# Kernel optimization log

Measured on AMD Instinct MI355X. Metric: run time of the kernel, lower is better.

The kernel has to match this reference:

```python
import jax, jax.numpy as jnp
import numpy as np

CLAMP_MIN, CLAMP_MAX = -3.0, 3.0
RANK = 16


def setup_inputs() -> dict:
    key = jax.random.key(0)
    ks = jax.random.split(key, 8)
    B, N, D, H, R = 8, 4096, 1024, 256, RANK
    s = 0.02  # small weight std so clamp/exp are well-conditioned
    return {
        "query_emb": jax.random.normal(ks[0], (B, D), jnp.float32),
        "context_embs": jax.random.normal(ks[1], (B, N, D), jnp.float32),
        "W1": jax.random.normal(ks[2], (D, H), jnp.float32) * s,
        "b1": jnp.zeros((H,), jnp.float32),
        "Wd": jax.random.normal(ks[3], (H, D), jnp.float32) * s,
        "bd": jnp.zeros((D,), jnp.float32),
        "WL": jax.random.normal(ks[4], (H, D * R), jnp.float32) * s,
        "bL": jnp.zeros((D * R,), jnp.float32),
        "Wdel": jax.random.normal(ks[5], (H, D), jnp.float32) * s,
        "bdel": jnp.zeros((D,), jnp.float32),
        "Wa": jax.random.normal(ks[6], (H, D), jnp.float32) * s,
        "ba": jnp.zeros((D,), jnp.float32),
    }


def reference(query_emb, context_embs, W1, b1, Wd, bd, WL, bL, Wdel, bdel, Wa, ba):
    B, N, D = context_embs.shape
    R = RANK
    # Backbone: Linear + ReLU (assumed MLP backbone)
    h = jax.nn.relu(query_emb @ W1 + b1)                      # (B,H)
    # Parameter heads (SkewGaussian.forward)
    log_d = jnp.clip(h @ Wd + bd, CLAMP_MIN, CLAMP_MAX)       # (B,D)
    L = (h @ WL + bL).reshape(B, D, R) * 0.1                  # (B,D,R)
    delta = (h @ Wdel + bdel) * 0.1                           # (B,D)
    alpha = h @ Wa + ba                                       # (B,D)

    mu = query_emb + delta                                    # (B,D)
    diff = context_embs - mu[:, None, :]                      # (B,N,D)
    d_inv = jnp.exp(-log_d)                                   # (B,D)

    # Diagonal Mahalanobis term
    mahal_diag = jnp.einsum('bnd,bd->bn', diff * diff, d_inv) # (B,N)

    # Woodbury correction with small RxR system per batch
    DinvL = d_inv[:, :, None] * L                             # (B,D,R)
    M = jnp.eye(R, dtype=L.dtype)[None] + jnp.einsum('bdr,bds->brs', L, DinvL)  # (B,R,R)
    M_inv = jnp.linalg.inv(M)
    v = diff * d_inv[:, None, :]                              # (B,N,D)
    w = jnp.einsum('bdr,bnd->brn', L, v)                      # (B,R,N)
    correction = jnp.sum(w * jnp.einsum('brs,bsn->brn', M_inv, w), axis=1)  # (B,N)

    mahal = mahal_diag - correction
    log_det = jnp.sum(log_d, axis=-1, keepdims=True) + jnp.linalg.slogdet(M)[1][:, None]  # (B,1)
    symmetric_score = -0.5 * (mahal + log_det)                # (B,N)

    skew_input = jnp.einsum('bd,bnd->bn', alpha, diff)
    skew_score = jax.nn.log_sigmoid(skew_input)
    return symmetric_score + skew_score
```

## Files before the change

### kernel.cpp

```cpp
#include <hip/hip_runtime.h>
#include <math.h>

#define BB 8
#define NN 4096
#define DD 1024
#define HH 256
#define RR 16

#define WS_GT      0
#define WS_MU      131072
#define WS_DINV    139264
#define WS_ALPHA   147456
#define WS_HP      155648
#define WS_LDP     188416
#define WS_MINV    188544
#define WS_LOGDET  190592
#define WS_L       190608

typedef __attribute__((address_space(3))) unsigned int lds_uint;
typedef __attribute__((address_space(1))) const unsigned int g_uint;

__global__ __launch_bounds__(256) void ka1_h(
    const float* __restrict__ qe, const float* __restrict__ W1, float* __restrict__ ws)
{
    const int b = blockIdx.x >> 4;
    const int sl = blockIdx.x & 15;
    const int c = threadIdx.x;
    __shared__ float qe_s[64];
    if (c < 64) qe_s[c] = qe[b * DD + sl * 64 + c];
    __syncthreads();
    float a0 = 0.f, a1 = 0.f, a2 = 0.f, a3 = 0.f;
    const float* W1p = W1 + (sl * 64) * HH;
    #pragma unroll 4
    for (int dl = 0; dl < 64; dl += 4) {
        a0 = fmaf(qe_s[dl + 0], W1p[(dl + 0) * HH + c], a0);
        a1 = fmaf(qe_s[dl + 1], W1p[(dl + 1) * HH + c], a1);
        a2 = fmaf(qe_s[dl + 2], W1p[(dl + 2) * HH + c], a2);
        a3 = fmaf(qe_s[dl + 3], W1p[(dl + 3) * HH + c], a3);
    }
    ws[WS_HP + (b * 16 + sl) * HH + c] = (a0 + a1) + (a2 + a3);
}

__global__ __launch_bounds__(256) void ka2_heads(
    const float* __restrict__ qe, const float* __restrict__ b1,
    const float* __restrict__ Wd, const float* __restrict__ bd,
    const float* __restrict__ WL, const float* __restrict__ bL,
    const float* __restrict__ Wdel, const float* __restrict__ bdel,
    const float* __restrict__ Wa, const float* __restrict__ ba,
    float* __restrict__ ws)
{
    __shared__ float h_s[BB * HH];
    __shared__ float red[4][512];
    const int tid = threadIdx.x;

    for (int i = tid; i < BB * HH; i += 256) {
        const int bb = i >> 8, c = i & 255;
        float v = b1[c];
        #pragma unroll
        for (int k = 0; k < 16; ++k) v += ws[WS_HP + (bb * 16 + k) * HH + c];
        h_s[i] = fmaxf(v, 0.f);
    }
    __syncthreads();

    const int blk = blockIdx.x;
    const int lane = tid & 63;
    const int u = tid >> 6;

    int mode; const float* W; const float* bias; int base;
    if (blk < 16)       { mode = 0; W = Wd;   bias = bd;   base = 0;  }
    else if (blk < 32)  { mode = 1; W = Wdel; bias = bdel; base = 16; }
    else if (blk < 48)  { mode = 2; W = Wa;   bias = ba;   base = 32; }
    else                { mode = 3; W = WL;   bias = bL;   base = 48; }
    const int ld = (mode == 3) ? (DD * RR) : DD;
    const int cc = (blk - base) * 64 + lane;

    float acc[8];
    #pragma unroll
    for (int b = 0; b < 8; ++b) acc[b] = 0.f;

    #pragma unroll 4
    for (int rr = 0; rr < 64; ++rr) {
        const int r = u * 64 + rr;
        const float wv = W[r * ld + cc];
        #pragma unroll
        for (int b = 0; b < 8; ++b) acc[b] = fmaf(h_s[b * HH + r], wv, acc[b]);
    }
    #pragma unroll
    for (int b = 0; b < 8; ++b) red[u][lane * 8 + b] = acc[b];
    __syncthreads();

    for (int e = tid; e < 512; e += 256) {
        const int cl = e >> 3, bb = e & 7;
        const int cm = (blk - base) * 64 + cl;
        float s = red[0][e] + red[1][e] + red[2][e] + red[3][e] + bias[cm];
        if (mode == 0) {
            const float ldv = fminf(fmaxf(s, -3.f), 3.f);
            ws[WS_DINV + bb * DD + cm] = expf(-ldv);
            red[0][e] = ldv;
        } else if (mode == 1) {
            ws[WS_MU + bb * DD + cm] = qe[bb * DD + cm] + 0.1f * s;
        } else if (mode == 2) {
            ws[WS_ALPHA + bb * DD + cm] = s;
        } else {
            ws[WS_L + bb * (DD * RR) + cm] = 0.1f * s;
        }
    }
    if (mode == 0) {
        __syncthreads();
        if (tid < 8) {
            float s = 0.f;
            for (int cl = 0; cl < 64; ++cl) s += red[0][cl * 8 + tid];
            ws[WS_LDP + blk * 8 + tid] = s;
        }
    }
}

__global__ __launch_bounds__(256) void kg_gt(float* __restrict__ ws)
{
    const int idx = blockIdx.x * 256 + threadIdx.x;
    const int d = idx & (DD - 1);
    const int r = (idx >> 10) & (RR - 1);
    const int b = idx >> 14;
    ws[WS_GT + idx] = ws[WS_DINV + b * DD + d] * ws[WS_L + (b * DD + d) * RR + r];
}

__global__ __launch_bounds__(1024) void kMGJ(float* __restrict__ ws)
{
    const int b = blockIdx.x;
    const int tid = threadIdx.x;
    const int dgr = tid >> 8;
    const int gs = tid & 255;
    const int g = gs >> 4, s = gs & 15;

    const float* Gt = ws + WS_GT + (size_t)b * (RR * DD);
    const float* Lp = ws + WS_L + (size_t)b * (DD * RR);

    float acc = 0.f;
    #pragma unroll 8
    for (int k = 0; k < 256; ++k) {
        const int d = dgr * 256 + k;
        acc = fmaf(Gt[g * DD + d], Lp[d * 16 + s], acc);
    }

    __shared__ float Mp[4][256];
    __shared__ float A[16][33];
    Mp[dgr][gs] = acc;
    __syncthreads();

    const bool act = (tid < 256);
    if (act) {
        A[g][s] = ((g == s) ? 1.f : 0.f) + Mp[0][gs] + Mp[1][gs] + Mp[2][gs] + Mp[3][gs];
        A[g][s + 16] = (g == s) ? 1.f : 0.f;
    }
    __syncthreads();

    float logdetM = 0.f;
    for (int k = 0; k < 16; ++k) {
        const float piv = A[k][k];
        if (tid == 0) logdetM += logf(piv);
        __syncthreads();
        if (act && g == k) {
            const float rinv = 1.f / piv;
            A[g][s] *= rinv;
            A[g][s + 16] *= rinv;
        }
        __syncthreads();
        const float f = (act && g != k) ? A[g][k] : 0.f;
        __syncthreads();
        if (act && g != k) {
            A[g][s]      = fmaf(-f, A[k][s],      A[g][s]);
            A[g][s + 16] = fmaf(-f, A[k][s + 16], A[g][s + 16]);
        }
        __syncthreads();
    }
    if (act) ws[WS_MINV + b * 256 + g * 16 + s] = A[g][s + 16];
    if (tid == 0) {
        float lds = 0.f;
        for (int k = 0; k < 16; ++k) lds += ws[WS_LDP + k * 8 + b];
        ws[WS_LOGDET + b] = lds + logdetM;
    }
}

__global__ __launch_bounds__(512, 2) void kc_main(
    const float* __restrict__ ctx, const float* __restrict__ ws, float* __restrict__ out)
{
    const int bid = blockIdx.x;
    const int b = bid >> 7;
    const int tile = bid & 127;
    const int tid = threadIdx.x;
    const int wave = tid >> 6;
    const int lane = tid & 63;
    const int n0 = tile * 32;

    __shared__ float gt_s[RR * DD];
    __shared__ float cbuf[2][32 * 64];

    {
        const float* gtg = ws + WS_GT + (size_t)b * (RR * DD);
        #pragma unroll
        for (int k = 0; k < 8; ++k) {
            __builtin_amdgcn_global_load_lds(
                (g_uint*)(gtg + (size_t)(k * 512 + wave * 64 + lane) * 4),
                (lds_uint*)((unsigned int*)gt_s + (k * 512 + wave * 64) * 4),
                16, 0, 0);
        }
        const int row = tid >> 4, f4 = tid & 15;
        const float* src = ctx + ((size_t)(b * NN + n0 + row)) * DD + (0 * 64) + ((f4 ^ (row & 7)) * 4);
        __builtin_amdgcn_global_load_lds(
            (g_uint*)src,
            (lds_uint*)((unsigned int*)&cbuf[0][0] + (wave * 64) * 4),
            16, 0, 0);
    }
    asm volatile("s_waitcnt vmcnt(0)" ::: "memory");
    __syncthreads();

    const int rl = lane >> 4;
    const int row_blk = wave * 4 + rl;
    const int f4 = lane & 15;
    const float4* gt4 = (const float4*)gt_s;
    const float4* mu4 = (const float4*)(ws + WS_MU + b * DD);
    const float4* dv4 = (const float4*)(ws + WS_DINV + b * DD);
    const float4* al4 = (const float4*)(ws + WS_ALPHA + b * DD);

    float g[16];
    #pragma unroll
    for (int r = 0; r < 16; ++r) g[r] = 0.f;
    float md = 0.f, aa = 0.f;

    const int stage_row = tid >> 4, stage_f4 = tid & 15;
    const float* stage_base = ctx + ((size_t)(b * NN + n0 + stage_row)) * DD + ((stage_f4 ^ (stage_row & 7)) * 4);

    for (int t = 0; t < 16; ++t) {
        if (t + 1 < 16) {
            __builtin_amdgcn_global_load_lds(
                (g_uint*)(stage_base + (t + 1) * 64),
                (lds_uint*)((unsigned int*)&cbuf[(t + 1) & 1][0] + (wave * 64) * 4),
                16, 0, 0);
            asm volatile("s_waitcnt vmcnt(1)" ::: "memory");
        } else {
            asm volatile("s_waitcnt vmcnt(0)" ::: "memory");
        }
        __syncthreads();

        const int fi = t * 16 + f4;
        const float4* cb4 = (const float4*)&cbuf[t & 1][0];
        const float4 cv = cb4[row_blk * 16 + (f4 ^ (row_blk & 7))];
        const float4 mv = mu4[fi];
        const float4 dvv = dv4[fi];
        const float4 av = al4[fi];

        const float d0 = cv.x - mv.x, d1 = cv.y - mv.y, d2 = cv.z - mv.z, d3 = cv.w - mv.w;
        md = fmaf(d0 * dvv.x, d0, md); md = fmaf(d1 * dvv.y, d1, md);
        md = fmaf(d2 * dvv.z, d2, md); md = fmaf(d3 * dvv.w, d3, md);
        aa = fmaf(av.x, d0, aa); aa = fmaf(av.y, d1, aa);
        aa = fmaf(av.z, d2, aa); aa = fmaf(av.w, d3, aa);

        #pragma unroll
        for (int r = 0; r < 16; ++r) {
            const float4 gt = gt4[r * 256 + fi];
            g[r] = fmaf(gt.x, d0, g[r]);
            g[r] = fmaf(gt.y, d1, g[r]);
            g[r] = fmaf(gt.z, d2, g[r]);
            g[r] = fmaf(gt.w, d3, g[r]);
        }
        __syncthreads();
    }

    float v[16];
    #pragma unroll
    for (int r = 0; r < 16; ++r) v[r] = g[r];

    #pragma unroll
    for (int s4 = 0; s4 < 4; ++s4) {
        const int m = 1 << s4;
        const int half = 8 >> s4;
        const bool up = (lane & m) != 0;
        #pragma unroll
        for (int ii = 0; ii < half; ++ii) {
            float x0 = v[2 * ii], x1 = v[2 * ii + 1];
            float y0 = __shfl_xor(x0, m, 64);
            float y1 = __shfl_xor(x1, m, 64);
            v[ii] = up ? (x1 + y1) : (x0 + y0);
        }
    }
    const float w = v[0];

    #pragma unroll
    for (int m = 1; m < 16; m <<= 1) {
        md += __shfl_xor(md, m, 64);
        aa += __shfl_xor(aa, m, 64);
    }

    const int r = lane & 15;
    const int base16 = lane & 48;
    const float* Minv = ws + WS_MINV + b * 256 + r * 16;
    float y = 0.f;
    #pragma unroll
    for (int s = 0; s < 16; ++s) y = fmaf(Minv[s], __shfl(w, base16 + s, 64), y);
    float corr = w * y;
    corr += __shfl_xor(corr, 1, 64);
    corr += __shfl_xor(corr, 2, 64);
    corr += __shfl_xor(corr, 4, 64);
    corr += __shfl_xor(corr, 8, 64);

    if (f4 == 0) {
        const float ld = ws[WS_LOGDET + b];
        const float lsig = fminf(aa, 0.f) - log1pf(expf(-fabsf(aa)));
        out[(size_t)b * NN + n0 + row_blk] = -0.5f * (md - corr + ld) + lsig;
    }
}

extern "C" void kernel_launch(void* const* d_in, const int* in_sizes, int n_in,
                              void* d_out, int out_size, void* d_ws, size_t ws_size,
                              hipStream_t stream)
{
    const float* qe   = (const float*)d_in[0];
    const float* ctx  = (const float*)d_in[1];
    const float* W1   = (const float*)d_in[2];
    const float* b1   = (const float*)d_in[3];
    const float* Wd   = (const float*)d_in[4];
    const float* bd   = (const float*)d_in[5];
    const float* WL   = (const float*)d_in[6];
    const float* bL   = (const float*)d_in[7];
    const float* Wdel = (const float*)d_in[8];
    const float* bdel = (const float*)d_in[9];
    const float* Wa   = (const float*)d_in[10];
    const float* ba   = (const float*)d_in[11];
    float* out = (float*)d_out;
    float* ws  = (float*)d_ws;

    ka1_h<<<128, 256, 0, stream>>>(qe, W1, ws);
    ka2_heads<<<304, 256, 0, stream>>>(qe, b1, Wd, bd, WL, bL, Wdel, bdel, Wa, ba, ws);
    kg_gt<<<512, 256, 0, stream>>>(ws);
    kMGJ<<<8, 1024, 0, stream>>>(ws);
    kc_main<<<1024, 512, 0, stream>>>(ctx, ws, out);
}
```

Before: 282.6 us.

## Register-block four context rows per thread and drop per-step block barriers

Each block now covers 128 context rows instead of 32, and each thread accumulates four rows at once. The 16 G^T float4 values loaded from LDS are reused across those four rows, cutting LDS traffic for G^T by a factor of four. Each wave now stages its own rows into a per-wave double buffer, so the per-step __syncthreads become per-wave vmcnt waits. mu, d_inv, alpha and M^-1 are cached in LDS. In exchange, register pressure rises (64 accumulators plus 16 float4), occupancy is limited to one block per CU, and the grid shrinks to 256 blocks, which may underfill the GPU.

```diff
diff --git a/kernel.cpp b/kernel.cpp
--- a/kernel.cpp
+++ b/kernel.cpp
@@ -181,132 +181,165 @@
     }
 }
 
-__global__ __launch_bounds__(512, 2) void kc_main(
+__global__ __launch_bounds__(512, 1) void kc_main(
     const float* __restrict__ ctx, const float* __restrict__ ws, float* __restrict__ out)
 {
     const int bid = blockIdx.x;
-    const int b = bid >> 7;
-    const int tile = bid & 127;
+    const int b = bid >> 5;
+    const int tile = bid & 31;
     const int tid = threadIdx.x;
     const int wave = tid >> 6;
     const int lane = tid & 63;
-    const int n0 = tile * 32;
+    const int slot = lane >> 4;
+    const int f4 = lane & 15;
+    const int n0 = tile * 128;
 
     __shared__ float gt_s[RR * DD];
-    __shared__ float cbuf[2][32 * 64];
+    __shared__ float prm_s[3 * DD];
+    __shared__ float minv_s[256];
+    __shared__ float cbuf[2][8][16][64];
 
     {
         const float* gtg = ws + WS_GT + (size_t)b * (RR * DD);
         #pragma unroll
-        for (int k = 0; k < 8; ++k) {
+        for (int k = 0; k < 8; ++k)
             __builtin_amdgcn_global_load_lds(
                 (g_uint*)(gtg + (size_t)(k * 512 + wave * 64 + lane) * 4),
                 (lds_uint*)((unsigned int*)gt_s + (k * 512 + wave * 64) * 4),
                 16, 0, 0);
-        }
-        const int row = tid >> 4, f4 = tid & 15;
-        const float* src = ctx + ((size_t)(b * NN + n0 + row)) * DD + (0 * 64) + ((f4 ^ (row & 7)) * 4);
-        __builtin_amdgcn_global_load_lds(
-            (g_uint*)src,
-            (lds_uint*)((unsigned int*)&cbuf[0][0] + (wave * 64) * 4),
-            16, 0, 0);
-    }
-    asm volatile("s_waitcnt vmcnt(0)" ::: "memory");
-    __syncthreads();
-
-    const int rl = lane >> 4;
-    const int row_blk = wave * 4 + rl;
-    const int f4 = lane & 15;
+        #pragma unroll
+        for (int i0 = 0; i0 < 2; ++i0) {
+            const int i = tid + i0 * 512;
+            if (i < 768) {
+                const int arr = i >> 8, off = i & 255;
+                ((float4*)prm_s)[arr * 256 + off] =
+                    *(const float4*)(ws + WS_MU + arr * 8192 + b * DD + off * 4);
+            }
+        }
+        if (tid < 256) minv_s[tid] = ws[WS_MINV + b * 256 + tid];
+    }
+    __syncthreads();
+
+    const float* srcp[4];
+    #pragma unroll
+    for (int j = 0; j < 4; ++j) {
+        const int rl = j * 4 + (lane >> 4);
+        srcp[j] = ctx + ((size_t)(b * NN + n0 + wave * 16 + rl)) * DD + ((lane & 15) ^ rl) * 4;
+    }
+
+    auto ISSUE = [&](int tt) {
+        float* dbase = &cbuf[tt & 1][wave][0][0];
+        #pragma unroll
+        for (int j = 0; j < 4; ++j)
+            __builtin_amdgcn_global_load_lds(
+                (g_uint*)(srcp[j] + tt * 64),
+                (lds_uint*)(dbase + j * 256),
+                16, 0, 0);
+    };
+
+    ISSUE(0);
+
     const float4* gt4 = (const float4*)gt_s;
-    const float4* mu4 = (const float4*)(ws + WS_MU + b * DD);
-    const float4* dv4 = (const float4*)(ws + WS_DINV + b * DD);
-    const float4* al4 = (const float4*)(ws + WS_ALPHA + b * DD);
-
-    float g[16];
-    #pragma unroll
-    for (int r = 0; r < 16; ++r) g[r] = 0.f;
-    float md = 0.f, aa = 0.f;
-
-    const int stage_row = tid >> 4, stage_f4 = tid & 15;
-    const float* stage_base = ctx + ((size_t)(b * NN + n0 + stage_row)) * DD + ((stage_f4 ^ (stage_row & 7)) * 4);
+    const float4* prm4 = (const float4*)prm_s;
+
+    float g[4][16];
+    float md[4], aa[4];
+    #pragma unroll
+    for (int k = 0; k < 4; ++k) {
+        md[k] = 0.f; aa[k] = 0.f;
+        #pragma unroll
+        for (int r = 0; r < 16; ++r) g[k][r] = 0.f;
+    }
 
     for (int t = 0; t < 16; ++t) {
-        if (t + 1 < 16) {
-            __builtin_amdgcn_global_load_lds(
-                (g_uint*)(stage_base + (t + 1) * 64),
-                (lds_uint*)((unsigned int*)&cbuf[(t + 1) & 1][0] + (wave * 64) * 4),
-                16, 0, 0);
-            asm volatile("s_waitcnt vmcnt(1)" ::: "memory");
-        } else {
-            asm volatile("s_waitcnt vmcnt(0)" ::: "memory");
-        }
-        __syncthreads();
-
-        const int fi = t * 16 + f4;
-        const float4* cb4 = (const float4*)&cbuf[t & 1][0];
-        const float4 cv = cb4[row_blk * 16 + (f4 ^ (row_blk & 7))];
-        const float4 mv = mu4[fi];
-        const float4 dvv = dv4[fi];
-        const float4 av = al4[fi];
-
-        const float d0 = cv.x - mv.x, d1 = cv.y - mv.y, d2 = cv.z - mv.z, d3 = cv.w - mv.w;
-        md = fmaf(d0 * dvv.x, d0, md); md = fmaf(d1 * dvv.y, d1, md);
-        md = fmaf(d2 * dvv.z, d2, md); md = fmaf(d3 * dvv.w, d3, md);
-        aa = fmaf(av.x, d0, aa); aa = fmaf(av.y, d1, aa);
-        aa = fmaf(av.z, d2, aa); aa = fmaf(av.w, d3, aa);
-
-        #pragma unroll
-        for (int r = 0; r < 16; ++r) {
-            const float4 gt = gt4[r * 256 + fi];
-            g[r] = fmaf(gt.x, d0, g[r]);
-            g[r] = fmaf(gt.y, d1, g[r]);
-            g[r] = fmaf(gt.z, d2, g[r]);
-            g[r] = fmaf(gt.w, d3, g[r]);
-        }
-        __syncthreads();
-    }
-
-    float v[16];
-    #pragma unroll
-    for (int r = 0; r < 16; ++r) v[r] = g[r];
-
-    #pragma unroll
-    for (int s4 = 0; s4 < 4; ++s4) {
-        const int m = 1 << s4;
-        const int half = 8 >> s4;
-        const bool up = (lane & m) != 0;
-        #pragma unroll
-        for (int ii = 0; ii < half; ++ii) {
-            float x0 = v[2 * ii], x1 = v[2 * ii + 1];
-            float y0 = __shfl_xor(x0, m, 64);
-            float y1 = __shfl_xor(x1, m, 64);
-            v[ii] = up ? (x1 + y1) : (x0 + y0);
-        }
-    }
-    const float w = v[0];
+        if (t + 1 < 16) ISSUE(t + 1);
+
+        const float4 mu = prm4[t * 16 + f4];
+        const float4 dv = prm4[256 + t * 16 + f4];
+        const float4 al = prm4[512 + t * 16 + f4];
+        float4 gtr[16];
+        #pragma unroll
+        for (int r = 0; r < 16; ++r) gtr[r] = gt4[r * 256 + t * 16 + f4];
+
+        if (t + 1 < 16) asm volatile("s_waitcnt vmcnt(4)" ::: "memory");
+        else            asm volatile("s_waitcnt vmcnt(0)" ::: "memory");
+        __builtin_amdgcn_sched_barrier(0);
+
+        const float4* cb = (const float4*)&cbuf[t & 1][wave][0][0];
+        #pragma unroll
+        for (int k = 0; k < 4; ++k) {
+            const int rl = slot * 4 + k;
+            const float4 cv = cb[rl * 16 + (f4 ^ rl)];
+            const float d0 = cv.x - mu.x, d1 = cv.y - mu.y, d2 = cv.z - mu.z, d3 = cv.w - mu.w;
+            md[k] = fmaf(d0 * dv.x, d0, md[k]); md[k] = fmaf(d1 * dv.y, d1, md[k]);
+            md[k] = fmaf(d2 * dv.z, d2, md[k]); md[k] = fmaf(d3 * dv.w, d3, md[k]);
+            aa[k] = fmaf(al.x, d0, aa[k]); aa[k] = fmaf(al.y, d1, aa[k]);
+            aa[k] = fmaf(al.z, d2, aa[k]); aa[k] = fmaf(al.w, d3, aa[k]);
+            #pragma unroll
+            for (int r = 0; r < 16; ++r) {
+                g[k][r] = fmaf(gtr[r].x, d0, g[k][r]);
+                g[k][r] = fmaf(gtr[r].y, d1, g[k][r]);
+                g[k][r] = fmaf(gtr[r].z, d2, g[k][r]);
+                g[k][r] = fmaf(gtr[r].w, d3, g[k][r]);
+            }
+        }
+    }
+
+    float w_[4];
+    #pragma unroll
+    for (int k = 0; k < 4; ++k) {
+        float v[16];
+        #pragma unroll
+        for (int r = 0; r < 16; ++r) v[r] = g[k][r];
+        #pragma unroll
+        for (int s4 = 0; s4 < 4; ++s4) {
+            const int m = 1 << s4;
+            const int half = 8 >> s4;
+            const bool up = (lane & m) != 0;
+            #pragma unroll
+            for (int ii = 0; ii < half; ++ii) {
+                float x0 = v[2 * ii], x1 = v[2 * ii + 1];
+                float y0 = __shfl_xor(x0, m, 64);
+                float y1 = __shfl_xor(x1, m, 64);
+                v[ii] = up ? (x1 + y1) : (x0 + y0);
+            }
+        }
+        w_[k] = v[0];
+    }
 
     #pragma unroll
     for (int m = 1; m < 16; m <<= 1) {
-        md += __shfl_xor(md, m, 64);
-        aa += __shfl_xor(aa, m, 64);
-    }
-
-    const int r = lane & 15;
+        #pragma unroll
+        for (int k = 0; k < 4; ++k) {
+            md[k] += __shfl_xor(md[k], m, 64);
+            aa[k] += __shfl_xor(aa[k], m, 64);
+        }
+    }
+
     const int base16 = lane & 48;
-    const float* Minv = ws + WS_MINV + b * 256 + r * 16;
-    float y = 0.f;
-    #pragma unroll
-    for (int s = 0; s < 16; ++s) y = fmaf(Minv[s], __shfl(w, base16 + s, 64), y);
-    float corr = w * y;
-    corr += __shfl_xor(corr, 1, 64);
-    corr += __shfl_xor(corr, 2, 64);
-    corr += __shfl_xor(corr, 4, 64);
-    corr += __shfl_xor(corr, 8, 64);
+    float corr[4];
+    #pragma unroll
+    for (int k = 0; k < 4; ++k) {
+        float y = 0.f;
+        #pragma unroll
+        for (int s = 0; s < 16; ++s)
+            y = fmaf(minv_s[s * 16 + f4], __shfl(w_[k], base16 + s, 64), y);
+        float c = w_[k] * y;
+        c += __shfl_xor(c, 1, 64);
+        c += __shfl_xor(c, 2, 64);
+        c += __shfl_xor(c, 4, 64);
+        c += __shfl_xor(c, 8, 64);
+        corr[k] = c;
+    }
 
     if (f4 == 0) {
         const float ld = ws[WS_LOGDET + b];
-        const float lsig = fminf(aa, 0.f) - log1pf(expf(-fabsf(aa)));
-        out[(size_t)b * NN + n0 + row_blk] = -0.5f * (md - corr + ld) + lsig;
+        #pragma unroll
+        for (int k = 0; k < 4; ++k) {
+            const float lsig = fminf(aa[k], 0.f) - log1pf(expf(-fabsf(aa[k])));
+            out[(size_t)b * NN + n0 + wave * 16 + slot * 4 + k] =
+                -0.5f * (md[k] - corr[k] + ld) + lsig;
+        }
     }
 }
 
@@ -333,5 +366,5 @@
     ka2_heads<<<304, 256, 0, stream>>>(qe, b1, Wd, bd, WL, bL, Wdel, bdel, Wa, ba, ws);
     kg_gt<<<512, 256, 0, stream>>>(ws);
     kMGJ<<<8, 1024, 0, stream>>>(ws);
-    kc_main<<<1024, 512, 0, stream>>>(ctx, ws, out);
-}
+    kc_main<<<256, 512, 0, stream>>>(ctx, ws, out);
+}
```

Result: no change. 282.2 us (-0.2%).
